# Performance work log

Hardware: AMD Instinct MI355X
Metric: run time of the kernel (lower is better)

## Reference

```python
import jax, jax.numpy as jnp
import numpy as np

B, N, DIN, DOUT, CHEB_K, EMBED = 64, 2048, 64, 64, 3, 16


def setup_inputs() -> dict:
    key = jax.random.key(0)
    k0, k1, k2, k3 = jax.random.split(key, 4)
    return {
        "x": jax.random.normal(k0, (B, N, DIN), dtype=jnp.float32),
        "node_embeddings": jax.random.normal(k1, (N, EMBED), dtype=jnp.float32),
        "weights_pool": jax.random.normal(k2, (EMBED, CHEB_K, DIN, DOUT), dtype=jnp.float32) * 0.02,
        "bias_pool": jax.random.normal(k3, (EMBED, DOUT), dtype=jnp.float32) * 0.02,
    }


def reference(x, node_embeddings, weights_pool, bias_pool):
    # x: (B, N, dim_in); node_embeddings: (N, embed_dim)
    n = node_embeddings.shape[0]
    # adaptive adjacency: softmax(relu(E E^T)) row-wise
    supports = jax.nn.softmax(jax.nn.relu(node_embeddings @ node_embeddings.T), axis=1)
    # Chebyshev polynomial basis: T0=I, T1=S, Tk = 2 S T_{k-1} - T_{k-2}
    tk = [jnp.eye(n, dtype=x.dtype), supports]
    for _ in range(2, CHEB_K):
        tk.append(2.0 * supports @ tk[-1] - tk[-2])
    S = jnp.stack(tk, axis=0)  # (K, N, N)
    # per-node weights/bias generated from embeddings
    weights = jnp.einsum('nd,dkio->nkio', node_embeddings, weights_pool)  # (N,K,din,dout)
    bias = node_embeddings @ bias_pool  # (N, dout)
    # graph conv: aggregate over neighbors for each Chebyshev order
    x_g = jnp.einsum('knm,bmc->bnkc', S, x)  # (B, N, K, din)
    out = jnp.einsum('bnki,nkio->bno', x_g, weights) + bias  # (B, N, dout)
    return out
```

## Files before the change

kernel.cpp:

```cpp
#include <hip/hip_runtime.h>
#include <hip/hip_bf16.h>

typedef unsigned short u16;
typedef short short8 __attribute__((ext_vector_type(8)));
typedef short short4v __attribute__((ext_vector_type(4)));
typedef float floatx4 __attribute__((ext_vector_type(4)));

#define NNODES 2048
#define BATCH  64
#define DIN    64
#define DOUT   64
#define EMB    16

__device__ __forceinline__ u16 f2bf(float f) {
  union { float f; unsigned u; } v; v.f = f;
  unsigned r = v.u + 0x7fffu + ((v.u >> 16) & 1u);
  return (u16)(r >> 16);
}

__device__ __forceinline__ void gload_lds16(const void* g, void* l) {
  __builtin_amdgcn_global_load_lds(
      (const __attribute__((address_space(1))) void*)g,
      (__attribute__((address_space(3))) void*)l, 16, 0, 0);
}

__global__ __launch_bounds__(256) void prologue(const float* __restrict__ E,
                                                const float* __restrict__ pool,
                                                const float* __restrict__ x,
                                                u16* __restrict__ Sb,
                                                u16* __restrict__ xtt,
                                                u16* __restrict__ W) {
  int bid = blockIdx.x;
  int t = threadIdx.x;

  if (bid < 768) {
    int ec = bid % 48, nc = bid / 48;
    int e = ec * 256 + t;
    int n0 = nc * 128;
    float pv[16];
#pragma unroll
    for (int d = 0; d < 16; d++) {
      float p = pool[(size_t)d * 12288 + e];
      if (e < 4096) p -= pool[(size_t)d * 12288 + 8192 + e];
      if (e >= 8192) p += p;
      pv[d] = p;
    }
    const float* er = E + (size_t)n0 * EMB;
#pragma unroll 4
    for (int nn = 0; nn < 128; nn++) {
      float acc = 0.0f;
#pragma unroll
      for (int d = 0; d < 16; d++) acc = fmaf(er[nn * EMB + d], pv[d], acc);
      W[(size_t)(n0 + nn) * 12288 + e] = f2bf(acc);
    }

  } else if (bid < 2816) {
    int n = bid - 768;
    const float4* ep = (const float4*)(E + (size_t)n * EMB);
    float4 e0 = ep[0], e1 = ep[1], e2 = ep[2], e3 = ep[3];
    float lg[8];
    float mx = 0.0f;
#pragma unroll
    for (int j = 0; j < 8; j++) {
      int m = t + j * 256;
      const float4* mp = (const float4*)(E + (size_t)m * EMB);
      float4 a = mp[0], b = mp[1], c = mp[2], d = mp[3];
      float dot = e0.x * a.x + e0.y * a.y + e0.z * a.z + e0.w * a.w
                + e1.x * b.x + e1.y * b.y + e1.z * b.z + e1.w * b.w
                + e2.x * c.x + e2.y * c.y + e2.z * c.z + e2.w * c.w
                + e3.x * d.x + e3.y * d.y + e3.z * d.z + e3.w * d.w;
      dot = fmaxf(dot, 0.0f);
      lg[j] = dot;
      mx = fmaxf(mx, dot);
    }
    __shared__ float smax[4], ssum[4];
#pragma unroll
    for (int off = 32; off > 0; off >>= 1) mx = fmaxf(mx, __shfl_xor(mx, off, 64));
    if ((t & 63) == 0) smax[t >> 6] = mx;
    __syncthreads();
    mx = fmaxf(fmaxf(smax[0], smax[1]), fmaxf(smax[2], smax[3]));
    float sum = 0.0f;
#pragma unroll
    for (int j = 0; j < 8; j++) {
      float e = __expf(lg[j] - mx);
      lg[j] = e;
      sum += e;
    }
#pragma unroll
    for (int off = 32; off > 0; off >>= 1) sum += __shfl_xor(sum, off, 64);
    if ((t & 63) == 0) ssum[t >> 6] = sum;
    __syncthreads();
    sum = ssum[0] + ssum[1] + ssum[2] + ssum[3];
    float inv = 1.0f / sum;
#pragma unroll
    for (int j = 0; j < 8; j++)
      Sb[(size_t)n * NNODES + t + j * 256] = f2bf(lg[j] * inv);

  } else {
    __shared__ float tile[64][68];
    int u = bid - 2816;
    int b = u >> 5;
    int m0 = (u & 31) * 64;
    int r = t >> 2, cs = (t & 3) * 16;
    const float* xp = x + ((size_t)b * NNODES + m0 + r) * DIN + cs;
    float4 v0 = ((const float4*)xp)[0];
    float4 v1 = ((const float4*)xp)[1];
    float4 v2 = ((const float4*)xp)[2];
    float4 v3 = ((const float4*)xp)[3];
    *(float4*)&tile[r][cs]      = v0;
    *(float4*)&tile[r][cs + 4]  = v1;
    *(float4*)&tile[r][cs + 8]  = v2;
    *(float4*)&tile[r][cs + 12] = v3;
    __syncthreads();
    int c = t >> 2, ms = (t & 3) * 16;
    short8 o0, o1;
#pragma unroll
    for (int j = 0; j < 8; j++) o0[j] = (short)f2bf(tile[ms + j][c]);
#pragma unroll
    for (int j = 0; j < 8; j++) o1[j] = (short)f2bf(tile[ms + 8 + j][c]);
    u16* op = xtt + ((size_t)b * 64 + c) * NNODES + m0 + ms;
    *(short8*)op = o0;
    *(short8*)(op + 8) = o1;
  }
}

#define GK 2048
#define GN 4096
#define NT 32
#define BUFU 24576

#define GEMM_PREAMBLE                                                          \
  __shared__ u16 smem[3 * BUFU];                                               \
  int t = threadIdx.x, lane = t & 63, wave = t >> 6;                           \
  int lin = blockIdx.y * gridDim.x + blockIdx.x;                               \
  int nwg = gridDim.x * gridDim.y;                                             \
  int sw = (lin & 7) * (nwg >> 3) + (lin >> 3);                                \
  int bx = sw & 31, by = sw >> 5;                                              \
  int m0 = by * 256, n0 = bx * 128;                                            \
  const u16* pg[6];                                                            \
  int lof[6];                                                                  \
  _Pragma("unroll") for (int j = 0; j < 4; j++) {                              \
    int c = t + 512 * j;                                                       \
    int row = c >> 3;                                                          \
    int gs = (c & 7) ^ (row & 7);                                              \
    pg[j] = A + (size_t)(m0 + row) * GK + gs * 8;                              \
    lof[j] = c * 8;                                                            \
  }                                                                            \
  _Pragma("unroll") for (int j = 0; j < 2; j++) {                              \
    int c = t + 512 * j;                                                       \
    int row = c >> 3;                                                          \
    int gs = (c & 7) ^ (row & 7);                                              \
    pg[4 + j] = Bt + (size_t)(n0 + row) * GK + gs * 8;                         \
    lof[4 + j] = 16384 + c * 8;                                                \
  }                                                                            \
  auto stage = [&](int b, int kt) {                                            \
    _Pragma("unroll") for (int j = 0; j < 6; j++)                              \
        gload_lds16(pg[j] + kt, &smem[b * BUFU + lof[j]]);                     \
  };                                                                           \
  int wr = wave >> 1, wc = wave & 1;                                           \
  int lr = lane & 15, lg = lane >> 4;                                          \
  floatx4 acc[4][4];                                                           \
  _Pragma("unroll") for (int mi = 0; mi < 4; mi++)                             \
      _Pragma("unroll") for (int ni = 0; ni < 4; ni++)                         \
          acc[mi][ni] = (floatx4)0.0f;                                         \
  int aoff[2][4], boff[2][4];                                                  \
  _Pragma("unroll") for (int s = 0; s < 2; s++) {                              \
    _Pragma("unroll") for (int mi = 0; mi < 4; mi++) {                         \
      int row = wr * 64 + mi * 16 + lr;                                        \
      int slot = s * 4 + lg;                                                   \
      aoff[s][mi] = row * 64 + (slot ^ (row & 7)) * 8;                         \
    }                                                                          \
    _Pragma("unroll") for (int ni = 0; ni < 4; ni++) {                         \
      int row = wc * 64 + ni * 16 + lr;                                        \
      int slot = s * 4 + lg;                                                   \
      boff[s][ni] = 16384 + row * 64 + (slot ^ (row & 7)) * 8;                 \
    }                                                                          \
  }                                                                            \
  auto compute = [&](int b) {                                                  \
    const u16* base = &smem[b * BUFU];                                         \
    short8 af[2][4], bf[2][4];                                                 \
    _Pragma("unroll") for (int s = 0; s < 2; s++) {                            \
      _Pragma("unroll") for (int mi = 0; mi < 4; mi++)                         \
          af[s][mi] = *(const short8*)(base + aoff[s][mi]);                    \
      _Pragma("unroll") for (int ni = 0; ni < 4; ni++)                         \
          bf[s][ni] = *(const short8*)(base + boff[s][ni]);                    \
    }                                                                          \
    _Pragma("unroll") for (int s = 0; s < 2; s++)                              \
        _Pragma("unroll") for (int mi = 0; mi < 4; mi++)                       \
            _Pragma("unroll") for (int ni = 0; ni < 4; ni++)                   \
                acc[mi][ni] = __builtin_amdgcn_mfma_f32_16x16x32_bf16(         \
                    af[s][mi], bf[s][ni], acc[mi][ni], 0, 0, 0);               \
  };                                                                           \
  stage(0, 0);                                                                 \
  stage(1, 64);                                                                \
  for (int tt = 0; tt < NT - 2; ++tt) {                                        \
    asm volatile("s_waitcnt vmcnt(6)" ::: "memory");                           \
    __builtin_amdgcn_s_barrier();                                              \
    stage((tt + 2) % 3, (tt + 2) * 64);                                        \
    compute(tt % 3);                                                           \
  }                                                                            \
  asm volatile("s_waitcnt vmcnt(6)" ::: "memory");                             \
  __builtin_amdgcn_s_barrier();                                                \
  compute((NT - 2) % 3);                                                       \
  asm volatile("s_waitcnt vmcnt(0)" ::: "memory");                             \
  __builtin_amdgcn_s_barrier();                                                \
  compute((NT - 1) % 3);                                                       \
  _Pragma("unroll") for (int mi = 0; mi < 4; mi++)                             \
      _Pragma("unroll") for (int ni = 0; ni < 4; ni++) {                       \
    int row = m0 + wr * 64 + mi * 16 + lg * 4;                                 \
    int col = n0 + wc * 64 + ni * 16 + lr;                                     \
    _Pragma("unroll") for (int r = 0; r < 4; r++)                              \
        C[(size_t)(row + r) * GN + col] = f2bf(acc[mi][ni][r]);                \
  }

__global__ __launch_bounds__(512) void gemm_plain(const u16* __restrict__ A,
                                                  const u16* __restrict__ Bt,
                                                  u16* __restrict__ C) {
  GEMM_PREAMBLE
}

__global__ __launch_bounds__(512) void gemm_tr(const u16* __restrict__ A,
                                               const u16* __restrict__ Bt,
                                               u16* __restrict__ C,
                                               u16* __restrict__ Ct) {
  GEMM_PREAMBLE
  __syncthreads();
  u16* scr = smem + wave * 4608;
#pragma unroll
  for (int mi = 0; mi < 4; mi++)
#pragma unroll
    for (int ni = 0; ni < 4; ni++) {
      int ncol = ni * 16 + lr;
      int chunk = mi * 2 + (lg >> 1);
      int off = ncol * 72 + chunk * 8 + (lg & 1) * 4;
      short4v sv;
#pragma unroll
      for (int r = 0; r < 4; r++) sv[r] = (short)f2bf(acc[mi][ni][r]);
      *(short4v*)&scr[off] = sv;
    }
  int c = lane;
  u16* op = Ct + (size_t)(n0 + wc * 64 + c) * GK + m0 + wr * 64;
#pragma unroll
  for (int jj = 0; jj < 8; jj++) {
    short8 v = *(const short8*)&scr[c * 72 + jj * 8];
    *(short8*)(op + jj * 8) = v;
  }
}

__global__ __launch_bounds__(256) void final_k(const float* __restrict__ x,
                                               const float* __restrict__ E,
                                               const float* __restrict__ bpool,
                                               const u16* __restrict__ xg1,
                                               const u16* __restrict__ xg2,
                                               const u16* __restrict__ W,
                                               float* __restrict__ out) {
  __shared__ u16 Xs[3][64][72];
  __shared__ u16 Ws[64 * 200];
  __shared__ float bias_s[64];
  int n = blockIdx.x, t = threadIdx.x;

  {
    int b = t >> 2, i0 = (t & 3) * 16;
    const float* xp = x + ((size_t)b * NNODES + n) * DIN + i0;
    float4 v0 = ((const float4*)xp)[0];
    float4 v1 = ((const float4*)xp)[1];
    float4 v2 = ((const float4*)xp)[2];
    float4 v3 = ((const float4*)xp)[3];
    u16* d = &Xs[0][b][i0];
    d[0] = f2bf(v0.x); d[1] = f2bf(v0.y); d[2] = f2bf(v0.z); d[3] = f2bf(v0.w);
    d[4] = f2bf(v1.x); d[5] = f2bf(v1.y); d[6] = f2bf(v1.z); d[7] = f2bf(v1.w);
    d[8] = f2bf(v2.x); d[9] = f2bf(v2.y); d[10] = f2bf(v2.z); d[11] = f2bf(v2.w);
    d[12] = f2bf(v3.x); d[13] = f2bf(v3.y); d[14] = f2bf(v3.z); d[15] = f2bf(v3.w);
  }
  for (int idx = t; idx < 512; idx += 256) {
    short8 v1 = *(const short8*)(xg1 + (size_t)n * 4096 + idx * 8);
    *(short8*)&Xs[1][idx >> 3][(idx & 7) * 8] = v1;
    short8 v2 = *(const short8*)(xg2 + (size_t)n * 4096 + idx * 8);
    *(short8*)&Xs[2][idx >> 3][(idx & 7) * 8] = v2;
  }
  for (int idx = t; idx < 1536; idx += 256) {
    short8 v = *(const short8*)(W + (size_t)n * 12288 + idx * 8);
    int kk = idx >> 3;
    int oo = (idx & 7) * 8;
    int c8 = kk >> 3, k7 = kk & 7;
#pragma unroll
    for (int j = 0; j < 8; j++) {
      int o = oo + j;
      Ws[o * 200 + ((c8 ^ (o >> 3)) << 3) + k7] = (u16)v[j];
    }
  }
  if (t < 64) {
    float acc = 0.0f;
#pragma unroll
    for (int d = 0; d < 16; d++)
      acc = fmaf(E[(size_t)n * EMB + d], bpool[d * 64 + t], acc);
    bias_s[t] = acc;
  }
  __syncthreads();

  int lane = t & 63, wave = t >> 6;
  int lr = lane & 15, lg = lane >> 4;
  int wb = wave * 16;
  floatx4 acc[4];
#pragma unroll
  for (int ot = 0; ot < 4; ot++) acc[ot] = (floatx4)0.0f;

#pragma unroll
  for (int ks = 0; ks < 6; ks++) {
    int kk = ks * 32 + lg * 8;
    int c8 = ks * 4 + lg;
    short8 a = *(const short8*)&Xs[kk >> 6][wb + lr][kk & 63];
#pragma unroll
    for (int ot = 0; ot < 4; ot++) {
      int o = ot * 16 + lr;
      short8 bb = *(const short8*)&Ws[o * 200 + ((c8 ^ (o >> 3)) << 3)];
      acc[ot] = __builtin_amdgcn_mfma_f32_16x16x32_bf16(a, bb, acc[ot], 0, 0, 0);
    }
  }
#pragma unroll
  for (int ot = 0; ot < 4; ot++) {
    int o = ot * 16 + lr;
    float bs = bias_s[o];
#pragma unroll
    for (int r = 0; r < 4; r++) {
      int b = wb + lg * 4 + r;
      out[((size_t)b * NNODES + n) * DOUT + o] = acc[ot][r] + bs;
    }
  }
}

extern "C" void kernel_launch(void* const* d_in, const int* in_sizes, int n_in,
                              void* d_out, int out_size, void* d_ws, size_t ws_size,
                              hipStream_t stream) {
  const float* x     = (const float*)d_in[0];
  const float* E     = (const float*)d_in[1];
  const float* pool  = (const float*)d_in[2];
  const float* bpool = (const float*)d_in[3];
  float* out = (float*)d_out;

  char* ws = (char*)d_ws;
  u16* Sb   = (u16*)(ws);
  u16* xtt  = (u16*)(ws + 8388608);
  u16* xg1  = (u16*)(ws + 25165824);
  u16* xg1t = (u16*)(ws + 41943040);
  u16* xg2  = (u16*)(ws + 58720256);
  u16* Wall = (u16*)(ws + 75497472);

  prologue<<<4864, 256, 0, stream>>>(E, pool, x, Sb, xtt, Wall);
  gemm_tr<<<dim3(32, 8), 512, 0, stream>>>(Sb, xtt, xg1, xg1t);
  gemm_plain<<<dim3(32, 8), 512, 0, stream>>>(Sb, xg1t, xg2);
  final_k<<<NNODES, 256, 0, stream>>>(x, E, bpool, xg1, xg2, Wall, out);
}
```

Baseline: 146.2 us.

## Split GEMM main loop into two interleaved phases with staged loads and priority

Splits each k-tile's compute into two half-phases over the N sub-tiles. Each phase issues its own part of the next tile's global-to-LDS loads, then waits on a barrier and raises wave priority around the MFMA block, in a ping-pong style schedule. The aim is to overlap memory issue with matrix math and keep fewer B fragments live in registers. In exchange it adds barriers per iteration and depends on pg/lof per-thread pointers that the stage helper is assumed to provide.

```diff
diff --git a/kernel.cpp b/kernel.cpp
--- a/kernel.cpp
+++ b/kernel.cpp
@@ -176,35 +176,49 @@
       boff[s][ni] = 16384 + row * 64 + (slot ^ (row & 7)) * 8;                 \
     }                                                                          \
   }                                                                            \
-  auto compute = [&](int b) {                                                  \
+  auto phase = [&](int b, int h, int bs, int kt, bool do_stage) {              \
     const u16* base = &smem[b * BUFU];                                         \
-    short8 af[2][4], bf[2][4];                                                 \
+    short8 afr[2][4], bfr[2][2];                                               \
     _Pragma("unroll") for (int s = 0; s < 2; s++) {                            \
       _Pragma("unroll") for (int mi = 0; mi < 4; mi++)                         \
-          af[s][mi] = *(const short8*)(base + aoff[s][mi]);                    \
-      _Pragma("unroll") for (int ni = 0; ni < 4; ni++)                         \
-          bf[s][ni] = *(const short8*)(base + boff[s][ni]);                    \
+          afr[s][mi] = *(const short8*)(base + aoff[s][mi]);                   \
+      _Pragma("unroll") for (int ni = 0; ni < 2; ni++)                         \
+          bfr[s][ni] = *(const short8*)(base + boff[s][h * 2 + ni]);           \
     }                                                                          \
+    if (do_stage) {                                                            \
+      _Pragma("unroll") for (int j = 0; j < 3; j++)                            \
+          gload_lds16(pg[h * 3 + j] + kt, &smem[bs * BUFU + lof[h * 3 + j]]);  \
+    }                                                                          \
+    __builtin_amdgcn_sched_barrier(0);                                         \
+    __builtin_amdgcn_s_barrier();                                              \
+    asm volatile("s_waitcnt lgkmcnt(0)" ::: "memory");                         \
+    __builtin_amdgcn_s_setprio(1);                                             \
     _Pragma("unroll") for (int s = 0; s < 2; s++)                              \
         _Pragma("unroll") for (int mi = 0; mi < 4; mi++)                       \
-            _Pragma("unroll") for (int ni = 0; ni < 4; ni++)                   \
-                acc[mi][ni] = __builtin_amdgcn_mfma_f32_16x16x32_bf16(         \
-                    af[s][mi], bf[s][ni], acc[mi][ni], 0, 0, 0);               \
+            _Pragma("unroll") for (int ni = 0; ni < 2; ni++)                   \
+                acc[mi][h * 2 + ni] = __builtin_amdgcn_mfma_f32_16x16x32_bf16( \
+                    afr[s][mi], bfr[s][ni], acc[mi][h * 2 + ni], 0, 0, 0);     \
+    __builtin_amdgcn_s_setprio(0);                                             \
   };                                                                           \
   stage(0, 0);                                                                 \
   stage(1, 64);                                                                \
   for (int tt = 0; tt < NT - 2; ++tt) {                                        \
     asm volatile("s_waitcnt vmcnt(6)" ::: "memory");                           \
     __builtin_amdgcn_s_barrier();                                              \
-    stage((tt + 2) % 3, (tt + 2) * 64);                                        \
-    compute(tt % 3);                                                           \
+    phase(tt % 3, 0, (tt + 2) % 3, (tt + 2) * 64, true);                       \
+    __builtin_amdgcn_s_barrier();                                              \
+    phase(tt % 3, 1, (tt + 2) % 3, (tt + 2) * 64, true);                       \
   }                                                                            \
   asm volatile("s_waitcnt vmcnt(6)" ::: "memory");                             \
   __builtin_amdgcn_s_barrier();                                                \
-  compute((NT - 2) % 3);                                                       \
+  phase((NT - 2) % 3, 0, 0, 0, false);                                         \
+  __builtin_amdgcn_s_barrier();                                                \
+  phase((NT - 2) % 3, 1, 0, 0, false);                                         \
   asm volatile("s_waitcnt vmcnt(0)" ::: "memory");                             \
   __builtin_amdgcn_s_barrier();                                                \
-  compute((NT - 1) % 3);                                                       \
+  phase((NT - 1) % 3, 0, 0, 0, false);                                         \
+  __builtin_amdgcn_s_barrier();                                                \
+  phase((NT - 1) % 3, 1, 0, 0, false);                                         \
   _Pragma("unroll") for (int mi = 0; mi < 4; mi++)                             \
       _Pragma("unroll") for (int ni = 0; ni < 4; ni++) {                       \
     int row = m0 + wr * 64 + mi * 16 + lg * 4;                                 \
```

Result: slower. 152.0 us (+3.9%).
